# Kernel tuning notes

Hardware: AMD Instinct MI355X
Metric: run time of the kernel (lower is better)

Reference implementation:

```python
import jax, jax.numpy as jnp
import numpy as np

N_NODES = 50000

def _gcn_layer(x, src, dst, W, b, n_nodes):
    # Linear transform first (PyG GCNConv): h = x @ W
    h = x @ W  # [N, out]
    # Add self-loops
    loop = jnp.arange(n_nodes, dtype=src.dtype)
    src2 = jnp.concatenate([src, loop])
    dst2 = jnp.concatenate([dst, loop])
    # Symmetric normalization deg^-1/2 (deg counts incoming edges incl. self-loop)
    deg = jax.ops.segment_sum(jnp.ones_like(dst2, dtype=h.dtype), dst2, num_segments=n_nodes)
    dinv = jnp.where(deg > 0, jax.lax.rsqrt(deg), 0.0)
    norm = dinv[src2] * dinv[dst2]  # [E+N]
    # Gather-scale-scatter aggregation
    msg = h[src2] * norm[:, None]  # [E+N, out]
    out = jax.ops.segment_sum(msg, dst2, num_segments=n_nodes)
    return out + b

def setup_inputs() -> dict:
    key = jax.random.key(0)
    k1, k2, k3, k4 = jax.random.split(key, 4)
    E = 800000
    x = jax.random.normal(k1, (N_NODES, 128), dtype=jnp.float32)
    edge_index = jax.random.randint(k2, (2, E), 0, N_NODES, dtype=jnp.int64)
    W1 = jax.random.normal(k3, (128, 512), dtype=jnp.float32) * (1.0 / np.sqrt(128))
    b1 = jnp.zeros((512,), dtype=jnp.float32)
    W2 = jax.random.normal(k4, (512, 250), dtype=jnp.float32) * (1.0 / np.sqrt(512))
    b2 = jnp.zeros((250,), dtype=jnp.float32)
    return {"x": x, "edge_index": edge_index, "W1": W1, "b1": b1, "W2": W2, "b2": b2}

def reference(x, edge_index, W1, b1, W2, b2):
    src, dst = edge_index[0], edge_index[1]
    h = _gcn_layer(x, src, dst, W1, b1, N_NODES)
    h = jax.nn.relu(h)
    h = _gcn_layer(h, src, dst, W2, b2, N_NODES)
    return jax.nn.relu(h)
```

## Files before the change

### kernel.cpp

```cpp
#include <hip/hip_runtime.h>

#define N_NODES 50000

typedef __attribute__((ext_vector_type(8))) short bf16x8;
typedef __attribute__((ext_vector_type(4))) float f32x4;

__device__ __forceinline__ ushort f2bf(float f) {
    union { float f; unsigned u; } v; v.f = f;
    unsigned r = v.u + 0x7fff + ((v.u >> 16) & 1);
    return (ushort)(r >> 16);
}
__device__ __forceinline__ float bf2f(ushort u) {
    union { unsigned u; float f; } v; v.u = ((unsigned)u) << 16;
    return v.f;
}
__device__ __forceinline__ float bf2f_lo(unsigned u) {
    union { unsigned u; float f; } v; v.u = u << 16;
    return v.f;
}
__device__ __forceinline__ float bf2f_hi(unsigned u) {
    union { unsigned u; float f; } v; v.u = u & 0xffff0000u;
    return v.f;
}

__global__ void k_detect(const void* ei, int* flag) {
    __shared__ int bad;
    if (threadIdx.x == 0) bad = 0;
    __syncthreads();
    long long v = ((const long long*)ei)[threadIdx.x];
    if (v < 0 || v >= N_NODES) atomicOr(&bad, 1);
    __syncthreads();
    if (threadIdx.x == 0) *flag = bad ? 0 : 1;
}

__device__ __forceinline__ int eload(const void* ei, int idx, int is64) {
    return is64 ? (int)((const long long*)ei)[idx] : ((const int*)ei)[idx];
}

__global__ void k_hist(const void* ei, const int* flag, int* deg, int e) {
    int i = blockIdx.x * blockDim.x + threadIdx.x;
    if (i >= e) return;
    int is64 = *flag;
    int d = eload(ei, e + i, is64);
    atomicAdd(&deg[d], 1);
}

__global__ __launch_bounds__(512)
void k_scanA(const int* __restrict__ deg, int* __restrict__ rp1,
             int* __restrict__ bsum, int n) {
    __shared__ int wsum[8];
    const int i = blockIdx.x * 512 + threadIdx.x;
    const int lane = threadIdx.x & 63, wid = threadIdx.x >> 6;
    int x = (i < n) ? deg[i] : 0;
    #pragma unroll
    for (int off = 1; off < 64; off <<= 1) {
        int y = __shfl_up(x, off, 64);
        if (lane >= off) x += y;
    }
    if (lane == 63) wsum[wid] = x;
    __syncthreads();
    if (wid == 0 && lane < 8) {
        int s = wsum[lane];
        #pragma unroll
        for (int off = 1; off < 8; off <<= 1) {
            int y = __shfl_up(s, off, 64);
            if (lane >= off) s += y;
        }
        wsum[lane] = s;
    }
    __syncthreads();
    int incl = x + (wid > 0 ? wsum[wid - 1] : 0);
    if (i < n) rp1[i] = incl;
    if (threadIdx.x == 0) bsum[blockIdx.x] = wsum[7];
}

__global__ void k_scanB(int* bsum, int nb) {
    __shared__ int ws2[2];
    const int lane = threadIdx.x & 63, wid = threadIdx.x >> 6;
    int x = (threadIdx.x < nb) ? bsum[threadIdx.x] : 0;
    #pragma unroll
    for (int off = 1; off < 64; off <<= 1) {
        int y = __shfl_up(x, off, 64);
        if (lane >= off) x += y;
    }
    if (lane == 63) ws2[wid] = x;
    __syncthreads();
    int incl = x + (wid > 0 ? ws2[0] : 0);
    if (threadIdx.x < nb) bsum[threadIdx.x] = incl;
}

__global__ __launch_bounds__(512)
void k_scanC(const int* __restrict__ deg, int* __restrict__ rowptr,
             const int* __restrict__ bsum, int* __restrict__ cur,
             float* __restrict__ dinv, int n) {
    const int i = blockIdx.x * 512 + threadIdx.x;
    if (i >= n) return;
    const int off = (blockIdx.x > 0) ? bsum[blockIdx.x - 1] : 0;
    const int d = deg[i];
    const int incl = rowptr[i + 1] + off;
    rowptr[i + 1] = incl;
    cur[i] = incl - d;
    dinv[i] = rsqrtf((float)(d + 1));
    if (i == 0) rowptr[0] = 0;
}

__global__ void k_fill(const void* ei, const int* flag, int* cur, int* adj, int e) {
    int i = blockIdx.x * blockDim.x + threadIdx.x;
    if (i >= e) return;
    int is64 = *flag;
    int s = eload(ei, i, is64);
    int d = eload(ei, e + i, is64);
    int pos = atomicAdd(&cur[d], 1);
    adj[pos] = s;
}

__global__ void k_splitT(const float* __restrict__ W, ushort* __restrict__ ohi,
                         ushort* __restrict__ olo, int R , int C ,
                         int Nout ) {
    int idx = blockIdx.x * blockDim.x + threadIdx.x;
    if (idx >= Nout * R) return;
    int n = idx / R;
    int k = idx - n * R;
    float v = (n < C) ? W[(size_t)k * C + n] : 0.0f;
    ushort hi = f2bf(v);
    ohi[idx] = hi;
    olo[idx] = f2bf(v - bf2f(hi));
}

__global__ __launch_bounds__(256)
void k_pull128v(const int* __restrict__ rowptr, const int* __restrict__ adj,
                const float* __restrict__ dinv, const float* __restrict__ x,
                ushort* __restrict__ ohi, int n) {
    const int i = blockIdx.x * 4 + (threadIdx.x >> 6);
    if (i >= n) return;
    const int lane = threadIdx.x & 63;
    const float2* x2 = (const float2*)x;
    const float di = dinv[i];
    float2 v = x2[(size_t)i * 64 + lane];
    float a0 = di * v.x, a1 = di * v.y;
    int j = rowptr[i];
    const int end = rowptr[i + 1];
    for (; j + 8 <= end; j += 8) {
        int s0 = adj[j],     s1 = adj[j + 1], s2 = adj[j + 2], s3 = adj[j + 3];
        int s4 = adj[j + 4], s5 = adj[j + 5], s6 = adj[j + 6], s7 = adj[j + 7];
        float w0 = dinv[s0], w1 = dinv[s1], w2 = dinv[s2], w3 = dinv[s3];
        float w4 = dinv[s4], w5 = dinv[s5], w6 = dinv[s6], w7 = dinv[s7];
        float2 p0 = x2[(size_t)s0 * 64 + lane];
        float2 p1 = x2[(size_t)s1 * 64 + lane];
        float2 p2 = x2[(size_t)s2 * 64 + lane];
        float2 p3 = x2[(size_t)s3 * 64 + lane];
        float2 p4 = x2[(size_t)s4 * 64 + lane];
        float2 p5 = x2[(size_t)s5 * 64 + lane];
        float2 p6 = x2[(size_t)s6 * 64 + lane];
        float2 p7 = x2[(size_t)s7 * 64 + lane];
        a0 += w0 * p0.x + w1 * p1.x + w2 * p2.x + w3 * p3.x;
        a1 += w0 * p0.y + w1 * p1.y + w2 * p2.y + w3 * p3.y;
        a0 += w4 * p4.x + w5 * p5.x + w6 * p6.x + w7 * p7.x;
        a1 += w4 * p4.y + w5 * p5.y + w6 * p6.y + w7 * p7.y;
    }
    for (; j + 4 <= end; j += 4) {
        int s0 = adj[j], s1 = adj[j + 1], s2 = adj[j + 2], s3 = adj[j + 3];
        float w0 = dinv[s0], w1 = dinv[s1], w2 = dinv[s2], w3 = dinv[s3];
        float2 p0 = x2[(size_t)s0 * 64 + lane];
        float2 p1 = x2[(size_t)s1 * 64 + lane];
        float2 p2 = x2[(size_t)s2 * 64 + lane];
        float2 p3 = x2[(size_t)s3 * 64 + lane];
        a0 += w0 * p0.x + w1 * p1.x + w2 * p2.x + w3 * p3.x;
        a1 += w0 * p0.y + w1 * p1.y + w2 * p2.y + w3 * p3.y;
    }
    for (; j < end; ++j) {
        int s = adj[j];
        float w = dinv[s];
        float2 p = x2[(size_t)s * 64 + lane];
        a0 += w * p.x;
        a1 += w * p.y;
    }
    a0 *= di; a1 *= di;
    ((unsigned*)ohi)[(size_t)i * 64 + lane] =
        (unsigned)f2bf(a0) | ((unsigned)f2bf(a1) << 16);
}

__global__ __launch_bounds__(256)
void k_pull250v(const int* __restrict__ rowptr, const int* __restrict__ adj,
                const float* __restrict__ dinv, const ushort* __restrict__ t,
                const float* __restrict__ bias, float* __restrict__ out, int n) {
    const int i = blockIdx.x * 4 + (threadIdx.x >> 6);
    if (i >= n) return;
    const int lane = threadIdx.x & 63;
    const uint2* t2 = (const uint2*)t;
    uint2 u = t2[(size_t)i * 64 + lane];
    float a0 = bf2f_lo(u.x), a1 = bf2f_hi(u.x);
    float a2 = bf2f_lo(u.y), a3 = bf2f_hi(u.y);
    int j = rowptr[i];
    const int end = rowptr[i + 1];
    for (; j + 8 <= end; j += 8) {
        int s0 = adj[j],     s1 = adj[j + 1], s2 = adj[j + 2], s3 = adj[j + 3];
        int s4 = adj[j + 4], s5 = adj[j + 5], s6 = adj[j + 6], s7 = adj[j + 7];
        uint2 u0 = t2[(size_t)s0 * 64 + lane];
        uint2 u1 = t2[(size_t)s1 * 64 + lane];
        uint2 u2 = t2[(size_t)s2 * 64 + lane];
        uint2 u3 = t2[(size_t)s3 * 64 + lane];
        uint2 u4 = t2[(size_t)s4 * 64 + lane];
        uint2 u5 = t2[(size_t)s5 * 64 + lane];
        uint2 u6 = t2[(size_t)s6 * 64 + lane];
        uint2 u7 = t2[(size_t)s7 * 64 + lane];
        a0 += bf2f_lo(u0.x) + bf2f_lo(u1.x) + bf2f_lo(u2.x) + bf2f_lo(u3.x);
        a1 += bf2f_hi(u0.x) + bf2f_hi(u1.x) + bf2f_hi(u2.x) + bf2f_hi(u3.x);
        a2 += bf2f_lo(u0.y) + bf2f_lo(u1.y) + bf2f_lo(u2.y) + bf2f_lo(u3.y);
        a3 += bf2f_hi(u0.y) + bf2f_hi(u1.y) + bf2f_hi(u2.y) + bf2f_hi(u3.y);
        a0 += bf2f_lo(u4.x) + bf2f_lo(u5.x) + bf2f_lo(u6.x) + bf2f_lo(u7.x);
        a1 += bf2f_hi(u4.x) + bf2f_hi(u5.x) + bf2f_hi(u6.x) + bf2f_hi(u7.x);
        a2 += bf2f_lo(u4.y) + bf2f_lo(u5.y) + bf2f_lo(u6.y) + bf2f_lo(u7.y);
        a3 += bf2f_hi(u4.y) + bf2f_hi(u5.y) + bf2f_hi(u6.y) + bf2f_hi(u7.y);
    }
    for (; j + 4 <= end; j += 4) {
        int s0 = adj[j], s1 = adj[j + 1], s2 = adj[j + 2], s3 = adj[j + 3];
        uint2 u0 = t2[(size_t)s0 * 64 + lane];
        uint2 u1 = t2[(size_t)s1 * 64 + lane];
        uint2 u2 = t2[(size_t)s2 * 64 + lane];
        uint2 u3 = t2[(size_t)s3 * 64 + lane];
        a0 += bf2f_lo(u0.x) + bf2f_lo(u1.x) + bf2f_lo(u2.x) + bf2f_lo(u3.x);
        a1 += bf2f_hi(u0.x) + bf2f_hi(u1.x) + bf2f_hi(u2.x) + bf2f_hi(u3.x);
        a2 += bf2f_lo(u0.y) + bf2f_lo(u1.y) + bf2f_lo(u2.y) + bf2f_lo(u3.y);
        a3 += bf2f_hi(u0.y) + bf2f_hi(u1.y) + bf2f_hi(u2.y) + bf2f_hi(u3.y);
    }
    for (; j < end; ++j) {
        uint2 us = t2[(size_t)adj[j] * 64 + lane];
        a0 += bf2f_lo(us.x); a1 += bf2f_hi(us.x);
        a2 += bf2f_lo(us.y); a3 += bf2f_hi(us.y);
    }
    const float d = dinv[i];
    const int c0 = lane * 4;
    if (lane < 62) {
        float2 b0 = *(const float2*)&bias[c0];
        float2 b1 = *(const float2*)&bias[c0 + 2];
        float2 o0, o1;
        o0.x = fmaxf(d * a0 + b0.x, 0.0f);
        o0.y = fmaxf(d * a1 + b0.y, 0.0f);
        o1.x = fmaxf(d * a2 + b1.x, 0.0f);
        o1.y = fmaxf(d * a3 + b1.y, 0.0f);
        *(float2*)&out[(size_t)i * 250 + c0] = o0;
        *(float2*)&out[(size_t)i * 250 + c0 + 2] = o1;
    } else if (lane == 62) {
        float2 b0 = *(const float2*)&bias[248];
        float2 o0;
        o0.x = fmaxf(d * a0 + b0.x, 0.0f);
        o0.y = fmaxf(d * a1 + b0.y, 0.0f);
        *(float2*)&out[(size_t)i * 250 + 248] = o0;
    }
}

__device__ __forceinline__ void gl16(const ushort* g, ushort* l) {
    __builtin_amdgcn_global_load_lds((const __attribute__((address_space(1))) void*)g,
                                     (__attribute__((address_space(3))) void*)l,
                                     16, 0, 0);
}

#define OFF_BH 4096
#define OFF_BL 12288
#define SMEM_HALF 20480

__global__ __launch_bounds__(256, 2)
void k_mfma(const ushort* __restrict__ A, const ushort* __restrict__ Bhi,
            const ushort* __restrict__ Blo, const float* __restrict__ bias,
            const float* __restrict__ rscale, ushort* __restrict__ outp,
            int M, int K, int ldc, int mode, int CX, int PY) {
    __shared__ __align__(16) ushort smem[2 * SMEM_HALF];

    int id = blockIdx.x;
    const int gsz = CX * 8;
    const int nfull = (PY >> 3) * gsz;
    int bx, by;
    if (id < nfull) {
        int gg = id / gsz;
        int r  = id - gg * gsz;
        bx = r >> 3;
        by = gg * 8 + (r & 7);
    } else {
        int rem  = id - nfull;
        int pbase = (PY >> 3) << 3;
        int prem  = PY - pbase;
        by = pbase + rem % prem;
        bx = rem / prem;
    }
    const int brow = by * 128;
    const int bcol = bx * 256;

    const int tid  = threadIdx.x;
    const int lane = tid & 63;
    const int w    = tid >> 6;
    const int g    = lane >> 4;
    const int lr   = lane & 15;

    auto STAGE = [&](ushort* buf, int k0) {
        const int kofs = k0 + w * 8;
        #pragma unroll
        for (int t2 = 0; t2 < 2; ++t2)
            gl16(A + (size_t)(brow + t2 * 64 + lane) * K + kofs,
                 buf + w * 1024 + t2 * 512);
        #pragma unroll
        for (int t4 = 0; t4 < 4; ++t4)
            gl16(Bhi + (size_t)(bcol + t4 * 64 + lane) * K + kofs,
                 buf + OFF_BH + w * 2048 + t4 * 512);
        #pragma unroll
        for (int t4 = 0; t4 < 4; ++t4)
            gl16(Blo + (size_t)(bcol + t4 * 64 + lane) * K + kofs,
                 buf + OFF_BL + w * 2048 + t4 * 512);
    };

    f32x4 acc[8][4] = {};

    auto COMPUTE = [&](const ushort* rb) {
        bf16x8 af[8], bh[4], bl[4];
        #pragma unroll
        for (int nt = 0; nt < 4; ++nt) {
            const int bo = g * 2048 + (w * 64 + nt * 16 + lr) * 8;
            bh[nt] = *(const bf16x8*)(rb + OFF_BH + bo);
            bl[nt] = *(const bf16x8*)(rb + OFF_BL + bo);
        }
        #pragma unroll
        for (int mt = 0; mt < 8; ++mt)
            af[mt] = *(const bf16x8*)(rb + g * 1024 + (mt * 16 + lr) * 8);
        #pragma unroll
        for (int mt = 0; mt < 8; ++mt)
            #pragma unroll
            for (int nt = 0; nt < 4; ++nt) {
                acc[mt][nt] = __builtin_amdgcn_mfma_f32_16x16x32_bf16(bh[nt], af[mt], acc[mt][nt], 0, 0, 0);
                acc[mt][nt] = __builtin_amdgcn_mfma_f32_16x16x32_bf16(bl[nt], af[mt], acc[mt][nt], 0, 0, 0);
            }
    };

    STAGE(smem, 0);
    int cur = 0;
    for (int k0 = 32; k0 < K; k0 += 32) {
        STAGE(smem + (cur ^ 1) * SMEM_HALF, k0);
        asm volatile("s_waitcnt vmcnt(10)" ::: "memory");
        __builtin_amdgcn_sched_barrier(0);
        __builtin_amdgcn_s_barrier();
        COMPUTE(smem + cur * SMEM_HALF);
        __builtin_amdgcn_sched_barrier(0);
        __builtin_amdgcn_s_barrier();
        cur ^= 1;
    }
    asm volatile("s_waitcnt vmcnt(0)" ::: "memory");
    __builtin_amdgcn_sched_barrier(0);
    __builtin_amdgcn_s_barrier();
    COMPUTE(smem + cur * SMEM_HALF);

    #pragma unroll
    for (int mt = 0; mt < 8; ++mt) {
        const int gr = brow + mt * 16 + lr;
        if (gr >= M) continue;
        const float rs = (mode == 0) ? rscale[gr] : 0.0f;
        #pragma unroll
        for (int nt = 0; nt < 4; ++nt) {
            const int gc0 = bcol + w * 64 + nt * 16 + g * 4;
            float v0, v1, v2, v3;
            if (mode == 0) {
                v0 = acc[mt][nt][0] * rs; v1 = acc[mt][nt][1] * rs;
                v2 = acc[mt][nt][2] * rs; v3 = acc[mt][nt][3] * rs;
            } else {
                const float4 bv = *(const float4*)&bias[gc0];
                v0 = fmaxf(acc[mt][nt][0] + bv.x, 0.0f);
                v1 = fmaxf(acc[mt][nt][1] + bv.y, 0.0f);
                v2 = fmaxf(acc[mt][nt][2] + bv.z, 0.0f);
                v3 = fmaxf(acc[mt][nt][3] + bv.w, 0.0f);
            }
            uint2 pk;
            pk.x = (unsigned)f2bf(v0) | ((unsigned)f2bf(v1) << 16);
            pk.y = (unsigned)f2bf(v2) | ((unsigned)f2bf(v3) << 16);
            *(uint2*)(outp + (size_t)gr * ldc + gc0) = pk;
        }
    }
}

extern "C" void kernel_launch(void* const* d_in, const int* in_sizes, int n_in,
                              void* d_out, int out_size, void* d_ws, size_t ws_size,
                              hipStream_t stream) {
    const float* x  = (const float*)d_in[0];
    const void*  ei = d_in[1];
    const float* W1 = (const float*)d_in[2];
    const float* b1 = (const float*)d_in[3];
    const float* W2 = (const float*)d_in[4];
    const float* b2 = (const float*)d_in[5];
    float* out = (float*)d_out;

    const int N = N_NODES;
    const int E = in_sizes[1] / 2;
    const int MPAD = 50048;
    const int NSCB = (N + 511) / 512;

    char* base = (char*)d_ws;
    int*   flag   = (int*)base;
    int*   deg    = (int*)(base + 256);
    int*   rowptr = deg + 51200;
    int*   cur    = rowptr + 51200;
    float* dinv   = (float*)(cur + 51200);
    int*   bsum   = (int*)(dinv + 51200);
    int*   adj    = bsum + 128;
    char*  p      = (char*)(adj + ((E + 63) & ~63));
    ushort* A1hi  = (ushort*)p;  p += (size_t)MPAD * 128 * 2;
    ushort* A1xx  = (ushort*)p;  p += (size_t)MPAD * 128 * 2;
    ushort* tbuf  = A1hi;
    ushort* h1hi  = (ushort*)p;  p += (size_t)MPAD * 512 * 2;
    ushort* Bt1hi = (ushort*)p;  p += 512 * 128 * 2;
    ushort* Bt1lo = (ushort*)p;  p += 512 * 128 * 2;
    ushort* Bt2hi = (ushort*)p;  p += 256 * 512 * 2;
    ushort* Bt2lo = (ushort*)p;  p += 256 * 512 * 2;
    (void)A1xx;

    k_detect<<<1, 1024, 0, stream>>>(ei, flag);
    hipMemsetAsync(deg, 0, (size_t)N * sizeof(int), stream);
    k_hist<<<(E + 255) / 256, 256, 0, stream>>>(ei, flag, deg, E);
    k_scanA<<<NSCB, 512, 0, stream>>>(deg, rowptr + 1, bsum, N);
    k_scanB<<<1, 128, 0, stream>>>(bsum, NSCB);
    k_scanC<<<NSCB, 512, 0, stream>>>(deg, rowptr, bsum, cur, dinv, N);
    k_fill<<<(E + 255) / 256, 256, 0, stream>>>(ei, flag, cur, adj, E);

    k_splitT<<<(512 * 128 + 255) / 256, 256, 0, stream>>>(W1, Bt1hi, Bt1lo, 128, 512, 512);
    k_splitT<<<(256 * 512 + 255) / 256, 256, 0, stream>>>(W2, Bt2hi, Bt2lo, 512, 250, 256);

    k_pull128v<<<(N + 3) / 4, 256, 0, stream>>>(rowptr, adj, dinv, x, A1hi, N);

    k_mfma<<<2 * 391, 256, 0, stream>>>(A1hi, Bt1hi, Bt1lo, b1, nullptr, h1hi,
                                        N, 128, 512, 1, 2, 391);

    k_mfma<<<1 * 391, 256, 0, stream>>>(h1hi, Bt2hi, Bt2lo, nullptr, dinv, tbuf,
                                        N, 512, 256, 0, 1, 391);

    k_pull250v<<<(N + 3) / 4, 256, 0, stream>>>(rowptr, adj, dinv, tbuf, b2, out, N);
}
```

Baseline: 326.9 us.

## Prescale x to bf16, merge small kernels, and process four edges per thread

Adds a k_scale pass that multiplies x by dinv and stores it as bf16, so the first-layer gather reads half the bytes and no longer loads dinv for each neighbour. Several launches are merged: the memset moves into the detect kernel, the block-sum scan is folded into k_scanC as a reduction over preceding block sums, and the two weight-split kernels become one. The histogram and CSR fill kernels now handle four edges per thread. The trade-off is an extra pass over x, lower precision in the gathered features, and a redundant reduction in every scan block.

```diff
diff --git a/kernel.cpp b/kernel.cpp
--- a/kernel.cpp
+++ b/kernel.cpp
@@ -23,26 +23,41 @@
     return v.f;
 }
 
-__global__ void k_detect(const void* ei, int* flag) {
-    __shared__ int bad;
-    if (threadIdx.x == 0) bad = 0;
-    __syncthreads();
-    long long v = ((const long long*)ei)[threadIdx.x];
-    if (v < 0 || v >= N_NODES) atomicOr(&bad, 1);
-    __syncthreads();
-    if (threadIdx.x == 0) *flag = bad ? 0 : 1;
-}
-
 __device__ __forceinline__ int eload(const void* ei, int idx, int is64) {
     return is64 ? (int)((const long long*)ei)[idx] : ((const int*)ei)[idx];
 }
 
+__global__ void k_init(const void* ei, int* flag, int* deg, int n) {
+    if (blockIdx.x == 0) {
+        __shared__ int bad;
+        if (threadIdx.x == 0) bad = 0;
+        __syncthreads();
+        long long v = ((const long long*)ei)[threadIdx.x];
+        if (v < 0 || v >= N_NODES) atomicOr(&bad, 1);
+        __syncthreads();
+        if (threadIdx.x == 0) *flag = bad ? 0 : 1;
+    }
+    int i = blockIdx.x * 256 + threadIdx.x;
+    if (i < n) deg[i] = 0;
+}
+
 __global__ void k_hist(const void* ei, const int* flag, int* deg, int e) {
-    int i = blockIdx.x * blockDim.x + threadIdx.x;
-    if (i >= e) return;
+    int base = (blockIdx.x * blockDim.x + threadIdx.x) * 4;
+    if (base >= e) return;
     int is64 = *flag;
-    int d = eload(ei, e + i, is64);
-    atomicAdd(&deg[d], 1);
+    if (base + 4 <= e) {
+        int d0 = eload(ei, e + base,     is64);
+        int d1 = eload(ei, e + base + 1, is64);
+        int d2 = eload(ei, e + base + 2, is64);
+        int d3 = eload(ei, e + base + 3, is64);
+        atomicAdd(&deg[d0], 1);
+        atomicAdd(&deg[d1], 1);
+        atomicAdd(&deg[d2], 1);
+        atomicAdd(&deg[d3], 1);
+    } else {
+        for (int i = base; i < e; ++i)
+            atomicAdd(&deg[eload(ei, e + i, is64)], 1);
+    }
 }
 
 __global__ __launch_bounds__(512)
@@ -74,28 +89,22 @@
     if (threadIdx.x == 0) bsum[blockIdx.x] = wsum[7];
 }
 
-__global__ void k_scanB(int* bsum, int nb) {
-    __shared__ int ws2[2];
-    const int lane = threadIdx.x & 63, wid = threadIdx.x >> 6;
-    int x = (threadIdx.x < nb) ? bsum[threadIdx.x] : 0;
-    #pragma unroll
-    for (int off = 1; off < 64; off <<= 1) {
-        int y = __shfl_up(x, off, 64);
-        if (lane >= off) x += y;
-    }
-    if (lane == 63) ws2[wid] = x;
-    __syncthreads();
-    int incl = x + (wid > 0 ? ws2[0] : 0);
-    if (threadIdx.x < nb) bsum[threadIdx.x] = incl;
-}
-
 __global__ __launch_bounds__(512)
 void k_scanC(const int* __restrict__ deg, int* __restrict__ rowptr,
              const int* __restrict__ bsum, int* __restrict__ cur,
-             float* __restrict__ dinv, int n) {
+             float* __restrict__ dinv, int n, int nb) {
+    __shared__ int spart[2];
+    if (threadIdx.x < 128) {
+        int v = (threadIdx.x < nb && (int)threadIdx.x < (int)blockIdx.x)
+                ? bsum[threadIdx.x] : 0;
+        #pragma unroll
+        for (int o = 32; o; o >>= 1) v += __shfl_down(v, o, 64);
+        if ((threadIdx.x & 63) == 0) spart[threadIdx.x >> 6] = v;
+    }
+    __syncthreads();
+    const int off = spart[0] + spart[1];
     const int i = blockIdx.x * 512 + threadIdx.x;
     if (i >= n) return;
-    const int off = (blockIdx.x > 0) ? bsum[blockIdx.x - 1] : 0;
     const int d = deg[i];
     const int incl = rowptr[i + 1] + off;
     rowptr[i + 1] = incl;
@@ -105,76 +114,105 @@
 }
 
 __global__ void k_fill(const void* ei, const int* flag, int* cur, int* adj, int e) {
-    int i = blockIdx.x * blockDim.x + threadIdx.x;
-    if (i >= e) return;
+    int base = (blockIdx.x * blockDim.x + threadIdx.x) * 4;
+    if (base >= e) return;
     int is64 = *flag;
-    int s = eload(ei, i, is64);
-    int d = eload(ei, e + i, is64);
-    int pos = atomicAdd(&cur[d], 1);
-    adj[pos] = s;
-}
-
-__global__ void k_splitT(const float* __restrict__ W, ushort* __restrict__ ohi,
-                         ushort* __restrict__ olo, int R , int C ,
-                         int Nout ) {
-    int idx = blockIdx.x * blockDim.x + threadIdx.x;
-    if (idx >= Nout * R) return;
-    int n = idx / R;
-    int k = idx - n * R;
-    float v = (n < C) ? W[(size_t)k * C + n] : 0.0f;
-    ushort hi = f2bf(v);
-    ohi[idx] = hi;
-    olo[idx] = f2bf(v - bf2f(hi));
+    if (base + 4 <= e) {
+        int s0 = eload(ei, base,     is64), d0 = eload(ei, e + base,     is64);
+        int s1 = eload(ei, base + 1, is64), d1 = eload(ei, e + base + 1, is64);
+        int s2 = eload(ei, base + 2, is64), d2 = eload(ei, e + base + 2, is64);
+        int s3 = eload(ei, base + 3, is64), d3 = eload(ei, e + base + 3, is64);
+        int p0 = atomicAdd(&cur[d0], 1);
+        int p1 = atomicAdd(&cur[d1], 1);
+        int p2 = atomicAdd(&cur[d2], 1);
+        int p3 = atomicAdd(&cur[d3], 1);
+        adj[p0] = s0;
+        adj[p1] = s1;
+        adj[p2] = s2;
+        adj[p3] = s3;
+    } else {
+        for (int i = base; i < e; ++i) {
+            int s = eload(ei, i, is64);
+            int d = eload(ei, e + i, is64);
+            adj[atomicAdd(&cur[d], 1)] = s;
+        }
+    }
+}
+
+__global__ void k_splitW(const float* __restrict__ W1, const float* __restrict__ W2,
+                         ushort* __restrict__ o1h, ushort* __restrict__ o1l,
+                         ushort* __restrict__ o2h, ushort* __restrict__ o2l) {
+    int idx = blockIdx.x * 256 + threadIdx.x;
+    if (idx < 512 * 128) {
+        int nn = idx >> 7, k = idx & 127;
+        float v = W1[(size_t)k * 512 + nn];
+        ushort hi = f2bf(v);
+        o1h[idx] = hi;
+        o1l[idx] = f2bf(v - bf2f(hi));
+    } else {
+        idx -= 512 * 128;
+        int nn = idx >> 9, k = idx & 511;
+        float v = (nn < 250) ? W2[(size_t)k * 250 + nn] : 0.0f;
+        ushort hi = f2bf(v);
+        o2h[idx] = hi;
+        o2l[idx] = f2bf(v - bf2f(hi));
+    }
 }
 
 __global__ __launch_bounds__(256)
-void k_pull128v(const int* __restrict__ rowptr, const int* __restrict__ adj,
-                const float* __restrict__ dinv, const float* __restrict__ x,
+void k_scale(const float* __restrict__ x, const float* __restrict__ dinv,
+             ushort* __restrict__ xs, int n) {
+    int idx = blockIdx.x * 256 + threadIdx.x;
+    if (idx >= n * 64) return;
+    int i = idx >> 6;
+    float2 v = ((const float2*)x)[idx];
+    float d = dinv[i];
+    ((unsigned*)xs)[idx] = (unsigned)f2bf(d * v.x) | ((unsigned)f2bf(d * v.y) << 16);
+}
+
+__global__ __launch_bounds__(256)
+void k_pull128b(const int* __restrict__ rowptr, const int* __restrict__ adj,
+                const float* __restrict__ dinv, const ushort* __restrict__ xs,
                 ushort* __restrict__ ohi, int n) {
     const int i = blockIdx.x * 4 + (threadIdx.x >> 6);
     if (i >= n) return;
     const int lane = threadIdx.x & 63;
-    const float2* x2 = (const float2*)x;
-    const float di = dinv[i];
-    float2 v = x2[(size_t)i * 64 + lane];
-    float a0 = di * v.x, a1 = di * v.y;
+    const unsigned* xs32 = (const unsigned*)xs;
+    unsigned u = xs32[(size_t)i * 64 + lane];
+    float a0 = bf2f_lo(u), a1 = bf2f_hi(u);
     int j = rowptr[i];
     const int end = rowptr[i + 1];
     for (; j + 8 <= end; j += 8) {
         int s0 = adj[j],     s1 = adj[j + 1], s2 = adj[j + 2], s3 = adj[j + 3];
         int s4 = adj[j + 4], s5 = adj[j + 5], s6 = adj[j + 6], s7 = adj[j + 7];
-        float w0 = dinv[s0], w1 = dinv[s1], w2 = dinv[s2], w3 = dinv[s3];
-        float w4 = dinv[s4], w5 = dinv[s5], w6 = dinv[s6], w7 = dinv[s7];
-        float2 p0 = x2[(size_t)s0 * 64 + lane];
-        float2 p1 = x2[(size_t)s1 * 64 + lane];
-        float2 p2 = x2[(size_t)s2 * 64 + lane];
-        float2 p3 = x2[(size_t)s3 * 64 + lane];
-        float2 p4 = x2[(size_t)s4 * 64 + lane];
-        float2 p5 = x2[(size_t)s5 * 64 + lane];
-        float2 p6 = x2[(size_t)s6 * 64 + lane];
-        float2 p7 = x2[(size_t)s7 * 64 + lane];
-        a0 += w0 * p0.x + w1 * p1.x + w2 * p2.x + w3 * p3.x;
-        a1 += w0 * p0.y + w1 * p1.y + w2 * p2.y + w3 * p3.y;
-        a0 += w4 * p4.x + w5 * p5.x + w6 * p6.x + w7 * p7.x;
-        a1 += w4 * p4.y + w5 * p5.y + w6 * p6.y + w7 * p7.y;
+        unsigned u0 = xs32[(size_t)s0 * 64 + lane];
+        unsigned u1 = xs32[(size_t)s1 * 64 + lane];
+        unsigned u2 = xs32[(size_t)s2 * 64 + lane];
+        unsigned u3 = xs32[(size_t)s3 * 64 + lane];
+        unsigned u4 = xs32[(size_t)s4 * 64 + lane];
+        unsigned u5 = xs32[(size_t)s5 * 64 + lane];
+        unsigned u6 = xs32[(size_t)s6 * 64 + lane];
+        unsigned u7 = xs32[(size_t)s7 * 64 + lane];
+        a0 += bf2f_lo(u0) + bf2f_lo(u1) + bf2f_lo(u2) + bf2f_lo(u3);
+        a1 += bf2f_hi(u0) + bf2f_hi(u1) + bf2f_hi(u2) + bf2f_hi(u3);
+        a0 += bf2f_lo(u4) + bf2f_lo(u5) + bf2f_lo(u6) + bf2f_lo(u7);
+        a1 += bf2f_hi(u4) + bf2f_hi(u5) + bf2f_hi(u6) + bf2f_hi(u7);
     }
     for (; j + 4 <= end; j += 4) {
         int s0 = adj[j], s1 = adj[j + 1], s2 = adj[j + 2], s3 = adj[j + 3];
-        float w0 = dinv[s0], w1 = dinv[s1], w2 = dinv[s2], w3 = dinv[s3];
-        float2 p0 = x2[(size_t)s0 * 64 + lane];
-        float2 p1 = x2[(size_t)s1 * 64 + lane];
-        float2 p2 = x2[(size_t)s2 * 64 + lane];
-        float2 p3 = x2[(size_t)s3 * 64 + lane];
-        a0 += w0 * p0.x + w1 * p1.x + w2 * p2.x + w3 * p3.x;
-        a1 += w0 * p0.y + w1 * p1.y + w2 * p2.y + w3 * p3.y;
+        unsigned u0 = xs32[(size_t)s0 * 64 + lane];
+        unsigned u1 = xs32[(size_t)s1 * 64 + lane];
+        unsigned u2 = xs32[(size_t)s2 * 64 + lane];
+        unsigned u3 = xs32[(size_t)s3 * 64 + lane];
+        a0 += bf2f_lo(u0) + bf2f_lo(u1) + bf2f_lo(u2) + bf2f_lo(u3);
+        a1 += bf2f_hi(u0) + bf2f_hi(u1) + bf2f_hi(u2) + bf2f_hi(u3);
     }
     for (; j < end; ++j) {
-        int s = adj[j];
-        float w = dinv[s];
-        float2 p = x2[(size_t)s * 64 + lane];
-        a0 += w * p.x;
-        a1 += w * p.y;
-    }
+        unsigned us = xs32[(size_t)adj[j] * 64 + lane];
+        a0 += bf2f_lo(us);
+        a1 += bf2f_hi(us);
+    }
+    const float di = dinv[i];
     a0 *= di; a1 *= di;
     ((unsigned*)ohi)[(size_t)i * 64 + lane] =
         (unsigned)f2bf(a0) | ((unsigned)f2bf(a1) << 16);
@@ -407,20 +445,20 @@
     ushort* Bt1lo = (ushort*)p;  p += 512 * 128 * 2;
     ushort* Bt2hi = (ushort*)p;  p += 256 * 512 * 2;
     ushort* Bt2lo = (ushort*)p;  p += 256 * 512 * 2;
+    ushort* xs    = (ushort*)p;  p += (size_t)MPAD * 128 * 2;
     (void)A1xx;
 
-    k_detect<<<1, 1024, 0, stream>>>(ei, flag);
-    hipMemsetAsync(deg, 0, (size_t)N * sizeof(int), stream);
-    k_hist<<<(E + 255) / 256, 256, 0, stream>>>(ei, flag, deg, E);
+    k_init<<<(N + 255) / 256, 256, 0, stream>>>(ei, flag, deg, N);
+    k_hist<<<(E / 4 + 255) / 256, 256, 0, stream>>>(ei, flag, deg, E);
     k_scanA<<<NSCB, 512, 0, stream>>>(deg, rowptr + 1, bsum, N);
-    k_scanB<<<1, 128, 0, stream>>>(bsum, NSCB);
-    k_scanC<<<NSCB, 512, 0, stream>>>(deg, rowptr, bsum, cur, dinv, N);
-    k_fill<<<(E + 255) / 256, 256, 0, stream>>>(ei, flag, cur, adj, E);
-
-    k_splitT<<<(512 * 128 + 255) / 256, 256, 0, stream>>>(W1, Bt1hi, Bt1lo, 128, 512, 512);
-    k_splitT<<<(256 * 512 + 255) / 256, 256, 0, stream>>>(W2, Bt2hi, Bt2lo, 512, 250, 256);
-
-    k_pull128v<<<(N + 3) / 4, 256, 0, stream>>>(rowptr, adj, dinv, x, A1hi, N);
+    k_scanC<<<NSCB, 512, 0, stream>>>(deg, rowptr, bsum, cur, dinv, N, NSCB);
+    k_fill<<<(E / 4 + 255) / 256, 256, 0, stream>>>(ei, flag, cur, adj, E);
+
+    k_splitW<<<(512 * 128 + 256 * 512) / 256, 256, 0, stream>>>(
+        W1, W2, Bt1hi, Bt1lo, Bt2hi, Bt2lo);
+    k_scale<<<(N * 64 + 255) / 256, 256, 0, stream>>>(x, dinv, xs, N);
+
+    k_pull128b<<<(N + 3) / 4, 256, 0, stream>>>(rowptr, adj, dinv, xs, A1hi, N);
 
     k_mfma<<<2 * 391, 256, 0, stream>>>(A1hi, Bt1hi, Bt1lo, b1, nullptr, h1hi,
                                         N, 128, 512, 1, 2, 391);
```

Result: faster. 306.2 us (-6.3%).
